# Performance work log

Hardware: AMD Instinct MI355X
Metric: run time of the kernel (lower is better)

Reference implementation:

```python
import jax, jax.numpy as jnp
import numpy as np

DIM = 1024
EPS_LN = 1e-5
EPS_MEM = 1e-6

def _layernorm(x, g, b):
    mu = jnp.mean(x, axis=-1, keepdims=True)
    var = jnp.mean((x - mu) ** 2, axis=-1, keepdims=True)
    return (x - mu) * jax.lax.rsqrt(var + EPS_LN) * g + b

def setup_inputs() -> dict:
    key = jax.random.key(0)
    ks = jax.random.split(key, 8)
    B, S, D = 4, 4096, DIM
    s1 = 1.0 / np.sqrt(D)
    s2 = 1.0 / np.sqrt(4 * D)
    return {
        "x": jax.random.normal(ks[0], (B, S, D), dtype=jnp.float32),
        "ln1_g": jnp.ones((D,), jnp.float32),
        "ln1_b": jnp.zeros((D,), jnp.float32),
        "ln2_g": jnp.ones((D,), jnp.float32),
        "ln2_b": jnp.zeros((D,), jnp.float32),
        "gate_w": jax.random.uniform(ks[1], (D, D), jnp.float32, -s1, s1),
        "gate_b": jax.random.uniform(ks[2], (D,), jnp.float32, -s1, s1),
        "value_w": jax.random.uniform(ks[3], (D, D), jnp.float32, -s1, s1),
        "value_b": jax.random.uniform(ks[4], (D,), jnp.float32, -s1, s1),
        "ffn_w1": jax.random.uniform(ks[5], (D, 4 * D), jnp.float32, -s1, s1),
        "ffn_b1": jnp.zeros((4 * D,), jnp.float32),
        "ffn_w2": jax.random.uniform(ks[6], (4 * D, D), jnp.float32, -s2, s2),
        "ffn_b2": jnp.zeros((D,), jnp.float32),
    }

def reference(x, ln1_g, ln1_b, ln2_g, ln2_b, gate_w, gate_b, value_w, value_b, ffn_w1, ffn_b1, ffn_w2, ffn_b2):
    h = _layernorm(x, ln1_g, ln1_b)
    g = jax.nn.sigmoid(h @ gate_w + gate_b)
    v = h @ value_w + value_b
    cumsum_v = jnp.cumsum(g * v, axis=1)
    cumsum_g = jnp.cumsum(g, axis=1) + EPS_MEM
    x = x + cumsum_v / cumsum_g
    h2 = _layernorm(x, ln2_g, ln2_b)
    ffn = jax.nn.gelu(h2 @ ffn_w1 + ffn_b1, approximate=False) @ ffn_w2 + ffn_b2
    return x + ffn
```

## Files before the change

kernel.cpp:

```cpp
#include <hip/hip_runtime.h>
#include <cstdint>
#include <cstddef>

#define D_MODEL 1024
#define SEQ     4096
#define BATCH   4
#define M_ROWS  (BATCH*SEQ)
#define NCHUNK  64
#define LCHUNK  (SEQ/NCHUNK)

typedef __bf16 bf16_t;
typedef __bf16 bf16x8 __attribute__((ext_vector_type(8)));
typedef __bf16 bf16x4 __attribute__((ext_vector_type(4)));
typedef float  f32x4  __attribute__((ext_vector_type(4)));

__device__ __forceinline__ void load_lds_128(const bf16_t* g, bf16_t* l) {
    __builtin_amdgcn_global_load_lds(
        (const __attribute__((address_space(1))) unsigned int*)g,
        (__attribute__((address_space(3))) unsigned int*)l,
        16, 0, 0);
}

__device__ __forceinline__ float2 bf16pair_to_f2(unsigned int u) {
    union { unsigned int i; float f; } a, b;
    a.i = u << 16;
    b.i = u & 0xffff0000u;
    float2 r; r.x = a.f; r.y = b.f; return r;
}

__global__ __launch_bounds__(256)
void transpose_to_bf16(const float* __restrict__ in, bf16_t* __restrict__ out,
                       int R, int C) {
    __shared__ float t[32][33];
    int tx = threadIdx.x & 31, ty = threadIdx.x >> 5;
    int c0 = blockIdx.x * 32, r0 = blockIdx.y * 32;
    #pragma unroll
    for (int j = 0; j < 32; j += 8)
        t[ty + j][tx] = in[(size_t)(r0 + ty + j) * C + c0 + tx];
    __syncthreads();
    #pragma unroll
    for (int j = 0; j < 32; j += 8)
        out[(size_t)(c0 + ty + j) * R + r0 + tx] = (bf16_t)t[tx][ty + j];
}

__global__ __launch_bounds__(256)
void ln_kernel(const float* __restrict__ x, const float* __restrict__ gamma,
               const float* __restrict__ beta, bf16_t* __restrict__ h) {
    int row = blockIdx.x;
    int tid = threadIdx.x;
    const float4* xr = (const float4*)(x + (size_t)row * D_MODEL);
    float4 v = xr[tid];
    float s  = v.x + v.y + v.z + v.w;
    float ss = v.x*v.x + v.y*v.y + v.z*v.z + v.w*v.w;
    #pragma unroll
    for (int off = 32; off; off >>= 1) {
        s  += __shfl_down(s, off);
        ss += __shfl_down(ss, off);
    }
    __shared__ float red[8];
    int wave = tid >> 6, lane = tid & 63;
    if (lane == 0) { red[wave] = s; red[4 + wave] = ss; }
    __syncthreads();
    if (tid == 0) {
        float S  = red[0] + red[1] + red[2] + red[3];
        float SS = red[4] + red[5] + red[6] + red[7];
        float mean = S * (1.0f / D_MODEL);
        float var  = SS * (1.0f / D_MODEL) - mean * mean;
        red[0] = mean;
        red[1] = rsqrtf(var + 1e-5f);
    }
    __syncthreads();
    float mean = red[0], rstd = red[1];
    float4 gv = ((const float4*)gamma)[tid];
    float4 bv = ((const float4*)beta)[tid];
    bf16x4 o;
    o[0] = (bf16_t)((v.x - mean) * rstd * gv.x + bv.x);
    o[1] = (bf16_t)((v.y - mean) * rstd * gv.y + bv.y);
    o[2] = (bf16_t)((v.z - mean) * rstd * gv.z + bv.z);
    o[3] = (bf16_t)((v.w - mean) * rstd * gv.w + bv.w);
    ((bf16x4*)h)[(size_t)row * (D_MODEL / 4) + tid] = o;
}

template <int MODE>
__global__ __launch_bounds__(256, 2)
void gemm_kernel(const bf16_t* __restrict__ A, const bf16_t* __restrict__ Bt,
                 const float* __restrict__ bias, const float* __restrict__ xres,
                 void* __restrict__ out, int M, int N, int K) {
    __shared__ __align__(16) bf16_t ldsA[128 * 32];
    __shared__ __align__(16) bf16_t ldsB[128 * 32];

    const int tid  = threadIdx.x;
    const int lane = tid & 63;
    const int wave = tid >> 6;
    const int wm   = wave & 1;
    const int wn   = wave >> 1;

    const int m0 = blockIdx.x * 128;
    const int n0 = blockIdx.y * 128;

    f32x4 acc[4][4];
    f32x4 zero = {0.f, 0.f, 0.f, 0.f};
    #pragma unroll
    for (int i = 0; i < 4; i++)
        #pragma unroll
        for (int j = 0; j < 4; j++) acc[i][j] = zero;

    const int rowInChunk = lane >> 2;
    const int colBlk     = (lane & 3) * 8;
    const int quad = lane >> 4;
    const int l16  = lane & 15;

    for (int k0 = 0; k0 < K; k0 += 32) {
        __syncthreads();
        #pragma unroll
        for (int r = 0; r < 2; r++) {
            int chunk = r * 4 + wave;
            int arow = m0 + chunk * 16 + rowInChunk;
            load_lds_128(A + (size_t)arow * K + k0 + colBlk,
                         ldsA + chunk * 512 + lane * 8);
            int brow = n0 + chunk * 16 + rowInChunk;
            load_lds_128(Bt + (size_t)brow * K + k0 + colBlk,
                         ldsB + chunk * 512 + lane * 8);
        }
        __syncthreads();

        bf16x8 af[4], bfr[4];
        #pragma unroll
        for (int mt = 0; mt < 4; mt++)
            af[mt] = *(const bf16x8*)(ldsA + (wm * 64 + mt * 16 + l16) * 32 + quad * 8);
        #pragma unroll
        for (int nt = 0; nt < 4; nt++)
            bfr[nt] = *(const bf16x8*)(ldsB + (wn * 64 + nt * 16 + l16) * 32 + quad * 8);
        #pragma unroll
        for (int mt = 0; mt < 4; mt++)
            #pragma unroll
            for (int nt = 0; nt < 4; nt++)
                acc[mt][nt] = __builtin_amdgcn_mfma_f32_16x16x32_bf16(
                    af[mt], bfr[nt], acc[mt][nt], 0, 0, 0);
    }

    #pragma unroll
    for (int mt = 0; mt < 4; mt++) {
        #pragma unroll
        for (int nt = 0; nt < 4; nt++) {
            int col = n0 + wn * 64 + nt * 16 + l16;
            float bv = bias[col];
            #pragma unroll
            for (int r = 0; r < 4; r++) {
                int row = m0 + wm * 64 + mt * 16 + quad * 4 + r;
                size_t oidx = (size_t)row * N + col;
                float val = acc[mt][nt][r] + bv;
                if (MODE == 0) {
                    val = 1.0f / (1.0f + __expf(-val));
                    ((bf16_t*)out)[oidx] = (bf16_t)val;
                } else if (MODE == 1) {
                    ((bf16_t*)out)[oidx] = (bf16_t)val;
                } else if (MODE == 2) {
                    val = 0.5f * val * (1.0f + erff(val * 0.70710678118654752f));
                    ((bf16_t*)out)[oidx] = (bf16_t)val;
                } else {
                    ((float*)out)[oidx] = xres[oidx] + val;
                }
            }
        }
    }
}

__global__ __launch_bounds__(256)
void scan_partial(const bf16_t* __restrict__ g, const bf16_t* __restrict__ v,
                  float* __restrict__ sg, float* __restrict__ sgv) {
    int dt = blockIdx.x & 1;
    int c  = (blockIdx.x >> 1) & (NCHUNK - 1);
    int b  = blockIdx.x >> 7;
    int d  = dt * 512 + threadIdx.x * 2;
    float s0 = 0.f, s1 = 0.f, t0 = 0.f, t1 = 0.f;
    for (int i = 0; i < LCHUNK; i++) {
        int s = c * LCHUNK + i;
        size_t idx = ((size_t)(b * SEQ + s)) * D_MODEL + d;
        float2 gf = bf16pair_to_f2(*(const unsigned int*)(g + idx));
        float2 vf = bf16pair_to_f2(*(const unsigned int*)(v + idx));
        s0 += gf.x; s1 += gf.y;
        t0 += gf.x * vf.x; t1 += gf.y * vf.y;
    }
    size_t o = ((size_t)(b * NCHUNK + c)) * D_MODEL + d;
    sg[o] = s0;  sg[o + 1] = s1;
    sgv[o] = t0; sgv[o + 1] = t1;
}

__global__ __launch_bounds__(256)
void scan_prefix(float* __restrict__ sg, float* __restrict__ sgv) {
    int gid = blockIdx.x * 256 + threadIdx.x;
    int b = gid >> 9;
    int d = (gid & 511) * 2;
    float rg0 = 0.f, rg1 = 0.f, rv0 = 0.f, rv1 = 0.f;
    for (int c = 0; c < NCHUNK; c++) {
        size_t o = ((size_t)(b * NCHUNK + c)) * D_MODEL + d;
        float a0 = sg[o], a1 = sg[o + 1];
        sg[o] = rg0; sg[o + 1] = rg1;
        rg0 += a0; rg1 += a1;
        float b0 = sgv[o], b1 = sgv[o + 1];
        sgv[o] = rv0; sgv[o + 1] = rv1;
        rv0 += b0; rv1 += b1;
    }
}

__global__ __launch_bounds__(256)
void scan_apply(const bf16_t* __restrict__ g, const bf16_t* __restrict__ v,
                const float* __restrict__ x, const float* __restrict__ sg,
                const float* __restrict__ sgv, float* __restrict__ out) {
    int dt = blockIdx.x & 1;
    int c  = (blockIdx.x >> 1) & (NCHUNK - 1);
    int b  = blockIdx.x >> 7;
    int d  = dt * 512 + threadIdx.x * 2;
    size_t o = ((size_t)(b * NCHUNK + c)) * D_MODEL + d;
    float rg0 = sg[o], rg1 = sg[o + 1];
    float rv0 = sgv[o], rv1 = sgv[o + 1];
    for (int i = 0; i < LCHUNK; i++) {
        int s = c * LCHUNK + i;
        size_t idx = ((size_t)(b * SEQ + s)) * D_MODEL + d;
        float2 gf = bf16pair_to_f2(*(const unsigned int*)(g + idx));
        float2 vf = bf16pair_to_f2(*(const unsigned int*)(v + idx));
        rv0 += gf.x * vf.x; rg0 += gf.x;
        rv1 += gf.y * vf.y; rg1 += gf.y;
        float2 xv = *(const float2*)(x + idx);
        float2 ov;
        ov.x = xv.x + rv0 / (rg0 + 1e-6f);
        ov.y = xv.y + rv1 / (rg1 + 1e-6f);
        *(float2*)(out + idx) = ov;
    }
}

extern "C" void kernel_launch(void* const* d_in, const int* in_sizes, int n_in,
                              void* d_out, int out_size, void* d_ws, size_t ws_size,
                              hipStream_t stream) {
    (void)in_sizes; (void)n_in; (void)out_size; (void)ws_size;
    const float* x       = (const float*)d_in[0];
    const float* ln1_g   = (const float*)d_in[1];
    const float* ln1_b   = (const float*)d_in[2];
    const float* ln2_g   = (const float*)d_in[3];
    const float* ln2_b   = (const float*)d_in[4];
    const float* gate_w  = (const float*)d_in[5];
    const float* gate_b  = (const float*)d_in[6];
    const float* value_w = (const float*)d_in[7];
    const float* value_b = (const float*)d_in[8];
    const float* ffn_w1  = (const float*)d_in[9];
    const float* ffn_b1  = (const float*)d_in[10];
    const float* ffn_w2  = (const float*)d_in[11];
    const float* ffn_b2  = (const float*)d_in[12];
    float* out = (float*)d_out;

    char* ws = (char*)d_ws;
    const size_t MB = 1024 * 1024;
    bf16_t* wg_t = (bf16_t*)(ws + 0 * MB);
    bf16_t* wv_t = (bf16_t*)(ws + 2 * MB);
    bf16_t* w1_t = (bf16_t*)(ws + 4 * MB);
    bf16_t* w2_t = (bf16_t*)(ws + 12 * MB);
    bf16_t* h    = (bf16_t*)(ws + 20 * MB);
    bf16_t* g    = (bf16_t*)(ws + 52 * MB);
    bf16_t* v    = (bf16_t*)(ws + 84 * MB);
    float*  sg   = (float*)(ws + 116 * MB);
    float*  sgv  = (float*)(ws + 117 * MB);
    bf16_t* act  = (bf16_t*)(ws + 118 * MB);

    transpose_to_bf16<<<dim3(32, 32), 256, 0, stream>>>(gate_w, wg_t, 1024, 1024);
    transpose_to_bf16<<<dim3(32, 32), 256, 0, stream>>>(value_w, wv_t, 1024, 1024);
    transpose_to_bf16<<<dim3(128, 32), 256, 0, stream>>>(ffn_w1, w1_t, 1024, 4096);
    transpose_to_bf16<<<dim3(32, 128), 256, 0, stream>>>(ffn_w2, w2_t, 4096, 1024);

    ln_kernel<<<M_ROWS, 256, 0, stream>>>(x, ln1_g, ln1_b, h);

    gemm_kernel<0><<<dim3(M_ROWS / 128, 1024 / 128), 256, 0, stream>>>(
        h, wg_t, gate_b, nullptr, g, M_ROWS, 1024, 1024);
    gemm_kernel<1><<<dim3(M_ROWS / 128, 1024 / 128), 256, 0, stream>>>(
        h, wv_t, value_b, nullptr, v, M_ROWS, 1024, 1024);

    scan_partial<<<BATCH * NCHUNK * 2, 256, 0, stream>>>(g, v, sg, sgv);
    scan_prefix<<<8, 256, 0, stream>>>(sg, sgv);
    scan_apply<<<BATCH * NCHUNK * 2, 256, 0, stream>>>(g, v, x, sg, sgv, out);

    ln_kernel<<<M_ROWS, 256, 0, stream>>>(out, ln2_g, ln2_b, h);

    gemm_kernel<2><<<dim3(M_ROWS / 128, 4096 / 128), 256, 0, stream>>>(
        h, w1_t, ffn_b1, nullptr, act, M_ROWS, 4096, 1024);

    gemm_kernel<3><<<dim3(M_ROWS / 128, 1024 / 128), 256, 0, stream>>>(
        act, w2_t, ffn_b2, out, out, M_ROWS, 1024, 4096);
}
```

Measured before the change: 707.0 us.

## Widen GEMM K-tile with swizzled LDS, fuse gate/value GEMMs and transposes

The GEMM now stages a 64-wide K tile per iteration in an XOR-swizzled LDS layout, which halves the barrier count and avoids LDS bank conflicts. It also swaps the MFMA operands so that each lane owns four consecutive columns, allowing vectorized bf16x4/float4 epilogue stores. The gate and value projections are merged into a single N=2048 GEMM launch, and the four weight transposes are merged into one launch. The separate scan_prefix kernel is removed, and each scan_apply block now sums the preceding chunk totals itself, trading redundant reads for one fewer launch.

```diff
diff --git a/kernel.cpp b/kernel.cpp
--- a/kernel.cpp
+++ b/kernel.cpp
@@ -29,18 +29,26 @@
 }
 
 __global__ __launch_bounds__(256)
-void transpose_to_bf16(const float* __restrict__ in, bf16_t* __restrict__ out,
-                       int R, int C) {
+void transpose_all(const float* __restrict__ gate_w, const float* __restrict__ value_w,
+                   const float* __restrict__ ffn_w1, const float* __restrict__ ffn_w2,
+                   bf16_t* __restrict__ wgv_t, bf16_t* __restrict__ w1_t,
+                   bf16_t* __restrict__ w2_t) {
+    int id = blockIdx.x;
+    const float* in; bf16_t* outp; int R, C, bx, by;
+    if (id < 1024)      { in = gate_w;  outp = wgv_t;               R = 1024; C = 1024; bx = id & 31;  by = id >> 5; }
+    else if (id < 2048) { id -= 1024; in = value_w; outp = wgv_t + 1024*1024; R = 1024; C = 1024; bx = id & 31;  by = id >> 5; }
+    else if (id < 6144) { id -= 2048; in = ffn_w1;  outp = w1_t;    R = 1024; C = 4096; bx = id & 127; by = id >> 7; }
+    else                { id -= 6144; in = ffn_w2;  outp = w2_t;    R = 4096; C = 1024; bx = id & 31;  by = id >> 5; }
     __shared__ float t[32][33];
     int tx = threadIdx.x & 31, ty = threadIdx.x >> 5;
-    int c0 = blockIdx.x * 32, r0 = blockIdx.y * 32;
+    int c0 = bx * 32, r0 = by * 32;
     #pragma unroll
     for (int j = 0; j < 32; j += 8)
         t[ty + j][tx] = in[(size_t)(r0 + ty + j) * C + c0 + tx];
     __syncthreads();
     #pragma unroll
     for (int j = 0; j < 32; j += 8)
-        out[(size_t)(c0 + ty + j) * R + r0 + tx] = (bf16_t)t[tx][ty + j];
+        outp[(size_t)(c0 + ty + j) * R + r0 + tx] = (bf16_t)t[tx][ty + j];
 }
 
 __global__ __launch_bounds__(256)
@@ -84,10 +92,12 @@
 template <int MODE>
 __global__ __launch_bounds__(256, 2)
 void gemm_kernel(const bf16_t* __restrict__ A, const bf16_t* __restrict__ Bt,
-                 const float* __restrict__ bias, const float* __restrict__ xres,
-                 void* __restrict__ out, int M, int N, int K) {
-    __shared__ __align__(16) bf16_t ldsA[128 * 32];
-    __shared__ __align__(16) bf16_t ldsB[128 * 32];
+                 const float* __restrict__ bias, const float* __restrict__ bias2,
+                 const float* __restrict__ xres,
+                 void* __restrict__ out, void* __restrict__ out2,
+                 int M, int N, int K) {
+    __shared__ __align__(16) bf16_t ldsA[128 * 64];
+    __shared__ __align__(16) bf16_t ldsB[128 * 64];
 
     const int tid  = threadIdx.x;
     const int lane = tid & 63;
@@ -105,62 +115,90 @@
         #pragma unroll
         for (int j = 0; j < 4; j++) acc[i][j] = zero;
 
-    const int rowInChunk = lane >> 2;
-    const int colBlk     = (lane & 3) * 8;
+    const int rl     = lane >> 3;
+    const int srcCol = ((lane & 7) ^ rl) * 8;
+
     const int quad = lane >> 4;
     const int l16  = lane & 15;
-
-    for (int k0 = 0; k0 < K; k0 += 32) {
+    const int rswz = l16 & 7;
+
+    for (int k0 = 0; k0 < K; k0 += 64) {
         __syncthreads();
         #pragma unroll
-        for (int r = 0; r < 2; r++) {
-            int chunk = r * 4 + wave;
-            int arow = m0 + chunk * 16 + rowInChunk;
-            load_lds_128(A + (size_t)arow * K + k0 + colBlk,
-                         ldsA + chunk * 512 + lane * 8);
-            int brow = n0 + chunk * 16 + rowInChunk;
-            load_lds_128(Bt + (size_t)brow * K + k0 + colBlk,
-                         ldsB + chunk * 512 + lane * 8);
+        for (int i = 0; i < 4; i++) {
+            int cb = i * 4 + wave;
+            int r  = cb * 8 + rl;
+            load_lds_128(A  + (size_t)(m0 + r) * K + k0 + srcCol,
+                         ldsA + cb * 512 + lane * 8);
+            load_lds_128(Bt + (size_t)(n0 + r) * K + k0 + srcCol,
+                         ldsB + cb * 512 + lane * 8);
         }
         __syncthreads();
 
-        bf16x8 af[4], bfr[4];
         #pragma unroll
-        for (int mt = 0; mt < 4; mt++)
-            af[mt] = *(const bf16x8*)(ldsA + (wm * 64 + mt * 16 + l16) * 32 + quad * 8);
-        #pragma unroll
-        for (int nt = 0; nt < 4; nt++)
-            bfr[nt] = *(const bf16x8*)(ldsB + (wn * 64 + nt * 16 + l16) * 32 + quad * 8);
-        #pragma unroll
-        for (int mt = 0; mt < 4; mt++)
+        for (int kk = 0; kk < 2; kk++) {
+            int pos = ((quad + 4 * kk) ^ rswz) * 8;
+            bf16x8 af[4], bfr[4];
+            #pragma unroll
+            for (int mt = 0; mt < 4; mt++)
+                af[mt] = *(const bf16x8*)(ldsA + (wm * 64 + mt * 16 + l16) * 64 + pos);
             #pragma unroll
             for (int nt = 0; nt < 4; nt++)
-                acc[mt][nt] = __builtin_amdgcn_mfma_f32_16x16x32_bf16(
-                    af[mt], bfr[nt], acc[mt][nt], 0, 0, 0);
+                bfr[nt] = *(const bf16x8*)(ldsB + (wn * 64 + nt * 16 + l16) * 64 + pos);
+            #pragma unroll
+            for (int mt = 0; mt < 4; mt++)
+                #pragma unroll
+                for (int nt = 0; nt < 4; nt++)
+                    acc[mt][nt] = __builtin_amdgcn_mfma_f32_16x16x32_bf16(
+                        bfr[nt], af[mt], acc[mt][nt], 0, 0, 0);
+        }
     }
 
     #pragma unroll
     for (int mt = 0; mt < 4; mt++) {
+        int row = m0 + wm * 64 + mt * 16 + l16;
         #pragma unroll
         for (int nt = 0; nt < 4; nt++) {
-            int col = n0 + wn * 64 + nt * 16 + l16;
-            float bv = bias[col];
-            #pragma unroll
-            for (int r = 0; r < 4; r++) {
-                int row = m0 + wm * 64 + mt * 16 + quad * 4 + r;
-                size_t oidx = (size_t)row * N + col;
-                float val = acc[mt][nt][r] + bv;
-                if (MODE == 0) {
-                    val = 1.0f / (1.0f + __expf(-val));
-                    ((bf16_t*)out)[oidx] = (bf16_t)val;
-                } else if (MODE == 1) {
-                    ((bf16_t*)out)[oidx] = (bf16_t)val;
-                } else if (MODE == 2) {
-                    val = 0.5f * val * (1.0f + erff(val * 0.70710678118654752f));
-                    ((bf16_t*)out)[oidx] = (bf16_t)val;
-                } else {
-                    ((float*)out)[oidx] = xres[oidx] + val;
+            int col = n0 + wn * 64 + nt * 16 + quad * 4;
+            f32x4 a = acc[mt][nt];
+            if (MODE == 4) {
+                bool isV = (n0 >= 1024);
+                int c1 = col & 1023;
+                float4 bv = *(const float4*)((isV ? bias2 : bias) + c1);
+                float4 val;
+                val.x = a[0] + bv.x; val.y = a[1] + bv.y;
+                val.z = a[2] + bv.z; val.w = a[3] + bv.w;
+                if (!isV) {
+                    val.x = 1.0f / (1.0f + __expf(-val.x));
+                    val.y = 1.0f / (1.0f + __expf(-val.y));
+                    val.z = 1.0f / (1.0f + __expf(-val.z));
+                    val.w = 1.0f / (1.0f + __expf(-val.w));
                 }
+                bf16x4 p;
+                p[0] = (bf16_t)val.x; p[1] = (bf16_t)val.y;
+                p[2] = (bf16_t)val.z; p[3] = (bf16_t)val.w;
+                bf16_t* o = (bf16_t*)(isV ? out2 : out);
+                *(bf16x4*)(o + (size_t)row * 1024 + c1) = p;
+            } else if (MODE == 2) {
+                float4 bv = *(const float4*)(bias + col);
+                float4 val;
+                val.x = a[0] + bv.x; val.y = a[1] + bv.y;
+                val.z = a[2] + bv.z; val.w = a[3] + bv.w;
+                val.x = 0.5f * val.x * (1.0f + erff(val.x * 0.70710678118654752f));
+                val.y = 0.5f * val.y * (1.0f + erff(val.y * 0.70710678118654752f));
+                val.z = 0.5f * val.z * (1.0f + erff(val.z * 0.70710678118654752f));
+                val.w = 0.5f * val.w * (1.0f + erff(val.w * 0.70710678118654752f));
+                bf16x4 p;
+                p[0] = (bf16_t)val.x; p[1] = (bf16_t)val.y;
+                p[2] = (bf16_t)val.z; p[3] = (bf16_t)val.w;
+                *(bf16x4*)((bf16_t*)out + (size_t)row * N + col) = p;
+            } else {
+                float4 bv = *(const float4*)(bias + col);
+                float4 xr = *(const float4*)(xres + (size_t)row * N + col);
+                float4 val;
+                val.x = xr.x + a[0] + bv.x; val.y = xr.y + a[1] + bv.y;
+                val.z = xr.z + a[2] + bv.z; val.w = xr.w + a[3] + bv.w;
+                *(float4*)((float*)out + (size_t)row * N + col) = val;
             }
         }
     }
@@ -188,23 +226,6 @@
 }
 
 __global__ __launch_bounds__(256)
-void scan_prefix(float* __restrict__ sg, float* __restrict__ sgv) {
-    int gid = blockIdx.x * 256 + threadIdx.x;
-    int b = gid >> 9;
-    int d = (gid & 511) * 2;
-    float rg0 = 0.f, rg1 = 0.f, rv0 = 0.f, rv1 = 0.f;
-    for (int c = 0; c < NCHUNK; c++) {
-        size_t o = ((size_t)(b * NCHUNK + c)) * D_MODEL + d;
-        float a0 = sg[o], a1 = sg[o + 1];
-        sg[o] = rg0; sg[o + 1] = rg1;
-        rg0 += a0; rg1 += a1;
-        float b0 = sgv[o], b1 = sgv[o + 1];
-        sgv[o] = rv0; sgv[o + 1] = rv1;
-        rv0 += b0; rv1 += b1;
-    }
-}
-
-__global__ __launch_bounds__(256)
 void scan_apply(const bf16_t* __restrict__ g, const bf16_t* __restrict__ v,
                 const float* __restrict__ x, const float* __restrict__ sg,
                 const float* __restrict__ sgv, float* __restrict__ out) {
@@ -212,9 +233,14 @@
     int c  = (blockIdx.x >> 1) & (NCHUNK - 1);
     int b  = blockIdx.x >> 7;
     int d  = dt * 512 + threadIdx.x * 2;
-    size_t o = ((size_t)(b * NCHUNK + c)) * D_MODEL + d;
-    float rg0 = sg[o], rg1 = sg[o + 1];
-    float rv0 = sgv[o], rv1 = sgv[o + 1];
+    float rg0 = 0.f, rg1 = 0.f, rv0 = 0.f, rv1 = 0.f;
+    for (int p = 0; p < c; p++) {
+        size_t o = ((size_t)(b * NCHUNK + p)) * D_MODEL + d;
+        float2 a  = *(const float2*)(sg + o);
+        float2 bb = *(const float2*)(sgv + o);
+        rg0 += a.x;  rg1 += a.y;
+        rv0 += bb.x; rv1 += bb.y;
+    }
     for (int i = 0; i < LCHUNK; i++) {
         int s = c * LCHUNK + i;
         size_t idx = ((size_t)(b * SEQ + s)) * D_MODEL + d;
@@ -251,38 +277,32 @@
 
     char* ws = (char*)d_ws;
     const size_t MB = 1024 * 1024;
-    bf16_t* wg_t = (bf16_t*)(ws + 0 * MB);
-    bf16_t* wv_t = (bf16_t*)(ws + 2 * MB);
-    bf16_t* w1_t = (bf16_t*)(ws + 4 * MB);
-    bf16_t* w2_t = (bf16_t*)(ws + 12 * MB);
-    bf16_t* h    = (bf16_t*)(ws + 20 * MB);
-    bf16_t* g    = (bf16_t*)(ws + 52 * MB);
-    bf16_t* v    = (bf16_t*)(ws + 84 * MB);
-    float*  sg   = (float*)(ws + 116 * MB);
-    float*  sgv  = (float*)(ws + 117 * MB);
-    bf16_t* act  = (bf16_t*)(ws + 118 * MB);
-
-    transpose_to_bf16<<<dim3(32, 32), 256, 0, stream>>>(gate_w, wg_t, 1024, 1024);
-    transpose_to_bf16<<<dim3(32, 32), 256, 0, stream>>>(value_w, wv_t, 1024, 1024);
-    transpose_to_bf16<<<dim3(128, 32), 256, 0, stream>>>(ffn_w1, w1_t, 1024, 4096);
-    transpose_to_bf16<<<dim3(32, 128), 256, 0, stream>>>(ffn_w2, w2_t, 4096, 1024);
+    bf16_t* wgv_t = (bf16_t*)(ws + 0 * MB);
+    bf16_t* w1_t  = (bf16_t*)(ws + 4 * MB);
+    bf16_t* w2_t  = (bf16_t*)(ws + 12 * MB);
+    bf16_t* h     = (bf16_t*)(ws + 20 * MB);
+    bf16_t* g     = (bf16_t*)(ws + 52 * MB);
+    bf16_t* v     = (bf16_t*)(ws + 84 * MB);
+    float*  sg    = (float*)(ws + 116 * MB);
+    float*  sgv   = (float*)(ws + 117 * MB);
+    bf16_t* act   = (bf16_t*)(ws + 118 * MB);
+
+    transpose_all<<<10240, 256, 0, stream>>>(gate_w, value_w, ffn_w1, ffn_w2,
+                                             wgv_t, w1_t, w2_t);
 
     ln_kernel<<<M_ROWS, 256, 0, stream>>>(x, ln1_g, ln1_b, h);
 
-    gemm_kernel<0><<<dim3(M_ROWS / 128, 1024 / 128), 256, 0, stream>>>(
-        h, wg_t, gate_b, nullptr, g, M_ROWS, 1024, 1024);
-    gemm_kernel<1><<<dim3(M_ROWS / 128, 1024 / 128), 256, 0, stream>>>(
-        h, wv_t, value_b, nullptr, v, M_ROWS, 1024, 1024);
+    gemm_kernel<4><<<dim3(M_ROWS / 128, 2048 / 128), 256, 0, stream>>>(
+        h, wgv_t, gate_b, value_b, nullptr, g, v, M_ROWS, 2048, 1024);
 
     scan_partial<<<BATCH * NCHUNK * 2, 256, 0, stream>>>(g, v, sg, sgv);
-    scan_prefix<<<8, 256, 0, stream>>>(sg, sgv);
     scan_apply<<<BATCH * NCHUNK * 2, 256, 0, stream>>>(g, v, x, sg, sgv, out);
 
     ln_kernel<<<M_ROWS, 256, 0, stream>>>(out, ln2_g, ln2_b, h);
 
     gemm_kernel<2><<<dim3(M_ROWS / 128, 4096 / 128), 256, 0, stream>>>(
-        h, w1_t, ffn_b1, nullptr, act, M_ROWS, 4096, 1024);
+        h, w1_t, ffn_b1, nullptr, nullptr, act, nullptr, M_ROWS, 4096, 1024);
 
     gemm_kernel<3><<<dim3(M_ROWS / 128, 1024 / 128), 256, 0, stream>>>(
-        act, w2_t, ffn_b2, out, out, M_ROWS, 1024, 4096);
-}
+        act, w2_t, ffn_b2, nullptr, out, out, nullptr, M_ROWS, 1024, 4096);
+}
```

After: 679.8 us. 1.04x faster.
